# Kernel optimization log

Measured on AMD Instinct MI355X. Metric: run time of the kernel, lower is better.

Reference implementation:

```python
import jax, jax.numpy as jnp
import numpy as np

N, D, NUM_CLASSES = 1024, 256, 10
EPS = 1e-12


def setup_inputs() -> dict:
    key = jax.random.key(0)
    k1, k2, k3, k4 = jax.random.split(key, 4)
    return {
        "fm_s": jax.random.normal(k1, (N, D), dtype=jnp.float32),
        "fm_t": jax.random.normal(k2, (N, D), dtype=jnp.float32),
        "logvar_s": jax.random.normal(k3, (N, D), dtype=jnp.float32),
        "targets": jax.random.randint(k4, (N,), 0, NUM_CLASSES, dtype=jnp.int64),
        "fusion_true": 0,  # False branch (no multi_index)
    }


def reference(fm_s, fm_t, logvar_s, targets, fusion_true):
    # pairwise squared diff scaled by per-row (student) variance: (N, N, D)
    diff2 = (fm_s[:, None, :] - fm_t[None, :, :]) ** 2
    inv_var_term = diff2 / (2.0 * jnp.exp(logvar_s)[:, None, :] + EPS)
    half_lv = 0.5 * logvar_s[:, None, :]
    lp = jax.nn.relu(inv_var_term + half_lv).sum(-1)   # (N, N)
    ln = jax.nn.relu(-inv_var_term - half_lv).sum(-1)  # (N, N)
    pos = (targets[:, None] == targets[None, :]).astype(fm_s.dtype)  # self_mask_pos
    neg = 1.0 - pos
    loss_pos = lp * pos / pos.sum(-1, keepdims=True)
    loss_neg = ln * neg / neg.sum(-1, keepdims=True)
    # fusion_true == False path
    return loss_pos.sum(-1).mean() + loss_neg.sum(-1).mean()
```

## Files before the change

kernel.cpp:

```cpp
#include <hip/hip_runtime.h>
#include <math.h>

#define NN   1024
#define DD   256
#define NCLS 10

#define TI 64
#define TJ 128
#define DC 32
#define DSPLIT 8
#define NBLK ((NN / TI) * (NN / TJ) * DSPLIT)

typedef float f32x2 __attribute__((ext_vector_type(2)));
typedef float f32x4 __attribute__((ext_vector_type(4)));

__global__ __launch_bounds__(256) void count_kernel(const long long* __restrict__ tgt,
                                                    int* __restrict__ counts) {
    __shared__ int c[NCLS];
    int tid = threadIdx.x;
    if (tid < NCLS) c[tid] = 0;
    __syncthreads();
    for (int k = tid; k < NN; k += 256) atomicAdd(&c[(int)tgt[k]], 1);
    __syncthreads();
    if (tid < NCLS) counts[tid] = c[tid];
}

__global__ __launch_bounds__(256) void pair_kernel(
    const float* __restrict__ fm_s, const float* __restrict__ fm_t,
    const float* __restrict__ lv, const long long* __restrict__ tgt,
    const int* __restrict__ counts, float* __restrict__ partials)
{
    __shared__ float Al[TI * DC];
    __shared__ float Bl[TI * DC];
    __shared__ float Vl[TI * DC];
    __shared__ float Fl[TJ * DC];

    const int bid  = blockIdx.x;
    const int tile = bid >> 3;
    const int kd   = bid & 7;
    const int i0   = (tile >> 3) * TI;
    const int j0   = (tile & 7) * TJ;
    const int doff = kd * DC;

    const int tid  = threadIdx.x;
    const int tx   = tid & 15;
    const int ty   = tid >> 4;
    const int lane = tid & 63;
    const int w    = tid >> 6;

    const int srow = tid >> 3;
    const int sq   = tid & 7;
#pragma unroll
    for (int p = 0; p < 4; ++p) {
        const int r = p * 32 + srow;
        f32x4 v = *(const f32x4*)&fm_t[(j0 + r) * DD + doff + sq * 4];
        const int phys = (sq + (r >> 3)) & 7;
        *(f32x4*)&Fl[r * DC + phys * 4] = v;
    }
#pragma unroll
    for (int p = 0; p < 2; ++p) {
        const int r = p * 32 + srow;
        const int g = (i0 + r) * DD + doff + sq * 4;
        f32x4 fs = *(const f32x4*)&fm_s[g];
        f32x4 l  = *(const f32x4*)&lv[g];
        f32x4 A, B, V;
#pragma unroll
        for (int e = 0; e < 4; ++e) {
            const float iv = 0.5f * __expf(-l[e]);
            const float fsiv = fs[e] * iv;
            A[e] = fmaf(fsiv, fs[e], 0.5f * l[e]);
            B[e] = -2.0f * fsiv;
            V[e] = iv;
        }
        const int phys = (sq + (r >> 2)) & 7;
        *(f32x4*)&Al[r * DC + phys * 4] = A;
        *(f32x4*)&Bl[r * DC + phys * 4] = B;
        *(f32x4*)&Vl[r * DC + phys * 4] = V;
    }

    const int* tgt32 = (const int*)tgt;
    int ti_r[4], tj_r[8];
    float wp_r[4], wn_r[4];
#pragma unroll
    for (int ri = 0; ri < 4; ++ri) {
        ti_r[ri] = tgt32[(i0 + ty * 4 + ri) * 2];
        const int cnt = counts[ti_r[ri]];
        wp_r[ri] = 1.0f / (float)cnt;
        wn_r[ri] = 1.0f / (float)(NN - cnt);
    }
#pragma unroll
    for (int rj = 0; rj < 8; ++rj) tj_r[rj] = tgt32[(j0 + tx * 8 + rj) * 2];

    __syncthreads();

    float s1[4][8], s2[4][8];
#pragma unroll
    for (int a = 0; a < 4; ++a)
#pragma unroll
        for (int b = 0; b < 8; ++b) { s1[a][b] = 0.f; s2[a][b] = 0.f; }

#pragma unroll
    for (int k = 0; k < 8; ++k) {
        const int iq = ((k + ty) & 7) * 4;
        const f32x4* pa = (const f32x4*)&Al[ty * 128 + iq];
        const f32x4* pb = (const f32x4*)&Bl[ty * 128 + iq];
        const f32x4* pv = (const f32x4*)&Vl[ty * 128 + iq];
        f32x4 fa[4], fb[4], fv[4];
#pragma unroll
        for (int r = 0; r < 4; ++r) {
            fa[r] = pa[r * 8];
            fb[r] = pb[r * 8];
            fv[r] = pv[r * 8];
        }
        const f32x4* pf = (const f32x4*)&Fl[tx * 256 + ((k + tx) & 7) * 4];
#pragma unroll
        for (int rj = 0; rj < 8; ++rj) {
            const f32x4 f = pf[rj * 8];
            const f32x2 f01 = f.lo, f23 = f.hi;
            const f32x2 g01 = f01 * f01, g23 = f23 * f23;
#pragma unroll
            for (int ri = 0; ri < 4; ++ri) {
                const f32x2 t01 = __builtin_elementwise_fma(g01, fv[ri].lo,
                                    __builtin_elementwise_fma(f01, fb[ri].lo, fa[ri].lo));
                const f32x2 t23 = __builtin_elementwise_fma(g23, fv[ri].hi,
                                    __builtin_elementwise_fma(f23, fb[ri].hi, fa[ri].hi));
                s1[ri][rj] += (t01.x + t01.y) + (t23.x + t23.y);
                s2[ri][rj] += (fabsf(t01.x) + fabsf(t01.y)) + (fabsf(t23.x) + fabsf(t23.y));
            }
        }
    }

    float csum = 0.f;
#pragma unroll
    for (int ri = 0; ri < 4; ++ri) {
#pragma unroll
        for (int rj = 0; rj < 8; ++rj) {
            const float lp = 0.5f * (s2[ri][rj] + s1[ri][rj]);
            const float ln = 0.5f * (s2[ri][rj] - s1[ri][rj]);
            csum += (ti_r[ri] == tj_r[rj]) ? lp * wp_r[ri] : ln * wn_r[ri];
        }
    }

#pragma unroll
    for (int off = 32; off > 0; off >>= 1) csum += __shfl_down(csum, off);
    __syncthreads();
    if (lane == 0) Al[w] = csum;
    __syncthreads();
    if (tid == 0) partials[bid] = (Al[0] + Al[1]) + (Al[2] + Al[3]);
}

__global__ __launch_bounds__(256) void finalize_kernel(const float* __restrict__ partials,
                                                       float* __restrict__ out) {
    __shared__ float red[256];
    const int tid = threadIdx.x;
    red[tid] = (partials[tid] + partials[tid + 256]) +
               (partials[tid + 512] + partials[tid + 768]);
    __syncthreads();
    for (int s = 128; s > 0; s >>= 1) {
        if (tid < s) red[tid] += red[tid + s];
        __syncthreads();
    }
    if (tid == 0) out[0] = red[0] * (1.0f / (float)NN);
}

extern "C" void kernel_launch(void* const* d_in, const int* in_sizes, int n_in,
                              void* d_out, int out_size, void* d_ws, size_t ws_size,
                              hipStream_t stream) {
    const float* fm_s    = (const float*)d_in[0];
    const float* fm_t    = (const float*)d_in[1];
    const float* lv      = (const float*)d_in[2];
    const long long* tgt = (const long long*)d_in[3];

    int*   counts   = (int*)d_ws;
    float* partials = (float*)((char*)d_ws + 64);

    hipLaunchKernelGGL(count_kernel, dim3(1), dim3(256), 0, stream, tgt, counts);
    hipLaunchKernelGGL(pair_kernel, dim3(NBLK), dim3(256), 0, stream,
                       fm_s, fm_t, lv, tgt, counts, partials);
    hipLaunchKernelGGL(finalize_kernel, dim3(1), dim3(256), 0, stream,
                       partials, (float*)d_out);
}
```

Before: 39.02 us.

## Restructure pair kernel: lanes span D with register-held rows, drop D-split

```diff
diff --git a/kernel.cpp b/kernel.cpp
--- a/kernel.cpp
+++ b/kernel.cpp
@@ -5,64 +5,65 @@
 #define DD   256
 #define NCLS 10
 
-#define TI 64
-#define TJ 128
-#define DC 32
-#define DSPLIT 8
-#define NBLK ((NN / TI) * (NN / TJ) * DSPLIT)
+#define TIB 16
+#define TJB 32
+#define MI  4
+#define NBI (NN / TIB)
+#define NBJ (NN / TJB)
+#define NBLK (NBI * NBJ)
 
 typedef float f32x2 __attribute__((ext_vector_type(2)));
 typedef float f32x4 __attribute__((ext_vector_type(4)));
 
 __global__ __launch_bounds__(256) void count_kernel(const long long* __restrict__ tgt,
-                                                    int* __restrict__ counts) {
+                                                    float* __restrict__ wtab) {
     __shared__ int c[NCLS];
     int tid = threadIdx.x;
     if (tid < NCLS) c[tid] = 0;
     __syncthreads();
     for (int k = tid; k < NN; k += 256) atomicAdd(&c[(int)tgt[k]], 1);
     __syncthreads();
-    if (tid < NCLS) counts[tid] = c[tid];
+    if (tid < NCLS) {
+        wtab[tid]      = 1.0f / (float)c[tid];
+        wtab[16 + tid] = 1.0f / (float)(NN - c[tid]);
+    }
 }
 
 __global__ __launch_bounds__(256) void pair_kernel(
     const float* __restrict__ fm_s, const float* __restrict__ fm_t,
     const float* __restrict__ lv, const long long* __restrict__ tgt,
-    const int* __restrict__ counts, float* __restrict__ partials)
+    const float* __restrict__ wtab, float* __restrict__ partials)
 {
-    __shared__ float Al[TI * DC];
-    __shared__ float Bl[TI * DC];
-    __shared__ float Vl[TI * DC];
-    __shared__ float Fl[TJ * DC];
+    __shared__ float Fl[TJB * DD];
+    __shared__ int   tjL[TJB];
+    __shared__ float redw[4];
 
     const int bid  = blockIdx.x;
-    const int tile = bid >> 3;
-    const int kd   = bid & 7;
-    const int i0   = (tile >> 3) * TI;
-    const int j0   = (tile & 7) * TJ;
-    const int doff = kd * DC;
+    const int i0   = (bid >> 5) * TIB;
+    const int j0   = (bid & (NBJ - 1)) * TJB;
 
     const int tid  = threadIdx.x;
-    const int tx   = tid & 15;
-    const int ty   = tid >> 4;
+    const int w    = tid >> 6;
     const int lane = tid & 63;
-    const int w    = tid >> 6;
 
-    const int srow = tid >> 3;
-    const int sq   = tid & 7;
 #pragma unroll
-    for (int p = 0; p < 4; ++p) {
-        const int r = p * 32 + srow;
-        f32x4 v = *(const f32x4*)&fm_t[(j0 + r) * DD + doff + sq * 4];
-        const int phys = (sq + (r >> 3)) & 7;
-        *(f32x4*)&Fl[r * DC + phys * 4] = v;
+    for (int p = 0; p < TJB / 4; ++p) {
+        const int r = w + p * 4;
+        *(f32x4*)&Fl[r * DD + lane * 4] =
+            *(const f32x4*)&fm_t[(j0 + r) * DD + lane * 4];
     }
+    const int* tgt32 = (const int*)tgt;
+    if (tid < TJB) tjL[tid] = tgt32[(j0 + tid) * 2];
+
+    f32x4 Av[MI], Bv[MI], Vv[MI];
+    int   ti_r[MI];
+    float we_r[MI], wn_r[MI];
 #pragma unroll
-    for (int p = 0; p < 2; ++p) {
-        const int r = p * 32 + srow;
-        const int g = (i0 + r) * DD + doff + sq * 4;
-        f32x4 fs = *(const f32x4*)&fm_s[g];
-        f32x4 l  = *(const f32x4*)&lv[g];
+    for (int r = 0; r < MI; ++r) {
+        const int row = i0 + w * MI + r;
+        const int g   = row * DD + lane * 4;
+        const f32x4 fs = *(const f32x4*)&fm_s[g];
+        const f32x4 l  = *(const f32x4*)&lv[g];
         f32x4 A, B, V;
 #pragma unroll
         for (int e = 0; e < 4; ++e) {
@@ -72,92 +73,69 @@
             B[e] = -2.0f * fsiv;
             V[e] = iv;
         }
-        const int phys = (sq + (r >> 2)) & 7;
-        *(f32x4*)&Al[r * DC + phys * 4] = A;
-        *(f32x4*)&Bl[r * DC + phys * 4] = B;
-        *(f32x4*)&Vl[r * DC + phys * 4] = V;
+        Av[r] = A; Bv[r] = B; Vv[r] = V;
+        const int t = tgt32[row * 2];
+        ti_r[r] = t;
+        we_r[r] = wtab[t];
+        wn_r[r] = wtab[16 + t];
     }
-
-    const int* tgt32 = (const int*)tgt;
-    int ti_r[4], tj_r[8];
-    float wp_r[4], wn_r[4];
-#pragma unroll
-    for (int ri = 0; ri < 4; ++ri) {
-        ti_r[ri] = tgt32[(i0 + ty * 4 + ri) * 2];
-        const int cnt = counts[ti_r[ri]];
-        wp_r[ri] = 1.0f / (float)cnt;
-        wn_r[ri] = 1.0f / (float)(NN - cnt);
-    }
-#pragma unroll
-    for (int rj = 0; rj < 8; ++rj) tj_r[rj] = tgt32[(j0 + tx * 8 + rj) * 2];
 
     __syncthreads();
 
-    float s1[4][8], s2[4][8];
+    f32x2 acc[MI];
 #pragma unroll
-    for (int a = 0; a < 4; ++a)
+    for (int r = 0; r < MI; ++r) acc[r] = (f32x2)(0.f);
+
+    const f32x2 zero2 = (f32x2)(0.f);
+
+#pragma unroll 2
+    for (int j = 0; j < TJB; ++j) {
+        const f32x4 f = *(const f32x4*)&Fl[j * DD + lane * 4];
+        const int  tj = tjL[j];
+        const f32x2 f01 = f.lo, f23 = f.hi;
+        const f32x2 g01 = f01 * f01, g23 = f23 * f23;
 #pragma unroll
-        for (int b = 0; b < 8; ++b) { s1[a][b] = 0.f; s2[a][b] = 0.f; }
-
-#pragma unroll
-    for (int k = 0; k < 8; ++k) {
-        const int iq = ((k + ty) & 7) * 4;
-        const f32x4* pa = (const f32x4*)&Al[ty * 128 + iq];
-        const f32x4* pb = (const f32x4*)&Bl[ty * 128 + iq];
-        const f32x4* pv = (const f32x4*)&Vl[ty * 128 + iq];
-        f32x4 fa[4], fb[4], fv[4];
-#pragma unroll
-        for (int r = 0; r < 4; ++r) {
-            fa[r] = pa[r * 8];
-            fb[r] = pb[r * 8];
-            fv[r] = pv[r * 8];
-        }
-        const f32x4* pf = (const f32x4*)&Fl[tx * 256 + ((k + tx) & 7) * 4];
-#pragma unroll
-        for (int rj = 0; rj < 8; ++rj) {
-            const f32x4 f = pf[rj * 8];
-            const f32x2 f01 = f.lo, f23 = f.hi;
-            const f32x2 g01 = f01 * f01, g23 = f23 * f23;
-#pragma unroll
-            for (int ri = 0; ri < 4; ++ri) {
-                const f32x2 t01 = __builtin_elementwise_fma(g01, fv[ri].lo,
-                                    __builtin_elementwise_fma(f01, fb[ri].lo, fa[ri].lo));
-                const f32x2 t23 = __builtin_elementwise_fma(g23, fv[ri].hi,
-                                    __builtin_elementwise_fma(f23, fb[ri].hi, fa[ri].hi));
-                s1[ri][rj] += (t01.x + t01.y) + (t23.x + t23.y);
-                s2[ri][rj] += (fabsf(t01.x) + fabsf(t01.y)) + (fabsf(t23.x) + fabsf(t23.y));
-            }
+        for (int r = 0; r < MI; ++r) {
+            f32x2 t01 = __builtin_elementwise_fma(g01, Vv[r].lo,
+                          __builtin_elementwise_fma(f01, Bv[r].lo, Av[r].lo));
+            f32x2 t23 = __builtin_elementwise_fma(g23, Vv[r].hi,
+                          __builtin_elementwise_fma(f23, Bv[r].hi, Av[r].hi));
+            f32x2 rp01 = __builtin_elementwise_max(t01, zero2);
+            f32x2 rp23 = __builtin_elementwise_max(t23, zero2);
+            f32x2 rn01 = rp01 - t01;
+            f32x2 rn23 = rp23 - t23;
+            const bool eq = (ti_r[r] == tj);
+            const float wa = eq ? we_r[r] : 0.0f;
+            const float wb = eq ? 0.0f : wn_r[r];
+            const f32x2 wav = (f32x2)(wa), wbv = (f32x2)(wb);
+            acc[r] = __builtin_elementwise_fma(rp01, wav, acc[r]);
+            acc[r] = __builtin_elementwise_fma(rp23, wav, acc[r]);
+            acc[r] = __builtin_elementwise_fma(rn01, wbv, acc[r]);
+            acc[r] = __builtin_elementwise_fma(rn23, wbv, acc[r]);
         }
     }
 
-    float csum = 0.f;
-#pragma unroll
-    for (int ri = 0; ri < 4; ++ri) {
-#pragma unroll
-        for (int rj = 0; rj < 8; ++rj) {
-            const float lp = 0.5f * (s2[ri][rj] + s1[ri][rj]);
-            const float ln = 0.5f * (s2[ri][rj] - s1[ri][rj]);
-            csum += (ti_r[ri] == tj_r[rj]) ? lp * wp_r[ri] : ln * wn_r[ri];
-        }
-    }
-
+    f32x2 m = (acc[0] + acc[1]) + (acc[2] + acc[3]);
+    float csum = m.x + m.y;
 #pragma unroll
     for (int off = 32; off > 0; off >>= 1) csum += __shfl_down(csum, off);
     __syncthreads();
-    if (lane == 0) Al[w] = csum;
+    if (lane == 0) redw[w] = csum;
     __syncthreads();
-    if (tid == 0) partials[bid] = (Al[0] + Al[1]) + (Al[2] + Al[3]);
+    if (tid == 0) partials[bid] = (redw[0] + redw[1]) + (redw[2] + redw[3]);
 }
 
 __global__ __launch_bounds__(256) void finalize_kernel(const float* __restrict__ partials,
                                                        float* __restrict__ out) {
     __shared__ float red[256];
     const int tid = threadIdx.x;
-    red[tid] = (partials[tid] + partials[tid + 256]) +
-               (partials[tid + 512] + partials[tid + 768]);
+    float s = 0.f;
+#pragma unroll
+    for (int k = 0; k < NBLK / 256; ++k) s += partials[tid + k * 256];
+    red[tid] = s;
     __syncthreads();
-    for (int s = 128; s > 0; s >>= 1) {
-        if (tid < s) red[tid] += red[tid + s];
+    for (int st = 128; st > 0; st >>= 1) {
+        if (tid < st) red[tid] += red[tid + st];
         __syncthreads();
     }
     if (tid == 0) out[0] = red[0] * (1.0f / (float)NN);
@@ -171,12 +149,12 @@
     const float* lv      = (const float*)d_in[2];
     const long long* tgt = (const long long*)d_in[3];
 
-    int*   counts   = (int*)d_ws;
-    float* partials = (float*)((char*)d_ws + 64);
+    float* wtab     = (float*)d_ws;
+    float* partials = (float*)((char*)d_ws + 256);
 
-    hipLaunchKernelGGL(count_kernel, dim3(1), dim3(256), 0, stream, tgt, counts);
+    hipLaunchKernelGGL(count_kernel, dim3(1), dim3(256), 0, stream, tgt, wtab);
     hipLaunchKernelGGL(pair_kernel, dim3(NBLK), dim3(256), 0, stream,
-                       fm_s, fm_t, lv, tgt, counts, partials);
+                       fm_s, fm_t, lv, tgt, wtab, partials);
     hipLaunchKernelGGL(finalize_kernel, dim3(1), dim3(256), 0, stream,
                        partials, (float*)d_out);
 }
```

Result: slower. 48.70 us (+24.8%).
